# Kernel tuning notes

Hardware: AMD Instinct MI355X
Metric: run time of the kernel (lower is better)

Reference implementation:

```python
import jax, jax.numpy as jnp
import numpy as np

SPAN = 128
STRIDE = 4
LQ = 2048
LKV = 512
H = 16
DQK = 64
DV = 64
DQ = 1024
DOUT = 1024
T = SPAN // STRIDE  # table depth (rows of the sparse QK table)


def _tables():
    # Static precomputation mirroring the torch __init__ meshgrid logic.
    row, col = np.meshgrid(np.arange(T), np.arange(LQ), indexing='ij')
    qi_col = np.ceil((col - (SPAN - 1)) / STRIDE).astype(np.int64) + row  # kv index per (r, j)
    qi_row = -STRIDE * qi_col + col
    valid = (qi_row >= 0) & (qi_row < SPAN) & (qi_col >= 0) & (qi_col < LKV)
    kidx = np.clip(qi_col, 0, LKV - 1)  # clipped gather index; invalid slots masked later
    return jnp.asarray(kidx), jnp.asarray(valid)

KIDX, VALID = _tables()  # both [T, LQ]


def setup_inputs() -> dict:
    key = jax.random.key(0)
    ks = jax.random.split(key, 7)
    s = 0.02
    return {
        'q': jax.random.normal(ks[0], (2, LQ, DQ), jnp.float32),
        'k': jax.random.normal(ks[1], (2, LKV, DQ), jnp.float32),
        'v': jax.random.normal(ks[2], (2, LKV, DQ), jnp.float32),
        'Wq': jax.random.normal(ks[3], (DQ, H * DQK), jnp.float32) * s,
        'Wk': jax.random.normal(ks[4], (DQ, H * DQK), jnp.float32) * s,
        'Wv': jax.random.normal(ks[5], (DQ, H * DV), jnp.float32) * s,
        'Wo': jax.random.normal(ks[6], (H * DV, DOUT), jnp.float32) * s,
    }


def reference(q, k, v, Wq, Wk, Wv, Wo):
    B = q.shape[0]
    Q = (q @ Wq).reshape(B, LQ, H, DQK).transpose(0, 2, 1, 3)    # [B,H,LQ,DQK]
    K = (k @ Wk).reshape(B, LKV, H, DQK).transpose(0, 2, 1, 3)   # [B,H,LKV,DQK]
    V = (v @ Wv).reshape(B, LKV, H, DV).transpose(0, 2, 1, 3)    # [B,H,LKV,DV]

    # Gather K/V by the strided-span index table: [B,H,T,LQ,d]
    Kg = K[:, :, KIDX, :]
    Vg = V[:, :, KIDX, :]

    scores = jnp.einsum('bhjd,bhtjd->bhtj', Q, Kg) / np.float32(np.sqrt(DQK))
    scores = jnp.where(VALID, scores, -jnp.inf)
    probs = jax.nn.softmax(scores, axis=2)          # softmax over table rows (dim 2 in torch)
    probs = jnp.where(VALID, probs, 0.0)

    O = jnp.einsum('bhtj,bhtjd->bhjd', probs, Vg)   # [B,H,LQ,DV]
    O = O.transpose(0, 2, 1, 3).reshape(B, LQ, H * DV)
    return O @ Wo
```

## Files before the change

kernel.cpp:

```cpp
#include <hip/hip_runtime.h>
#include <hip/hip_bf16.h>

typedef __bf16 bf16x8 __attribute__((ext_vector_type(8)));
typedef float  f32x4  __attribute__((ext_vector_type(4)));
typedef unsigned short u16;
typedef unsigned int   u32;

__device__ __forceinline__ u16 f2b(float x) {
  __bf16 b = (__bf16)x;
  return __builtin_bit_cast(u16, b);
}

__device__ __forceinline__ void gload_lds16(const u16* g, u16* l) {
  __builtin_amdgcn_global_load_lds(
      (const __attribute__((address_space(1))) void*)g,
      (__attribute__((address_space(3))) void*)l, 16, 0, 0);
}

__device__ __forceinline__ void cvt8_store(u16* dst, float4 a, float4 b) {
  union { u16 u[8]; uint4 v; } r;
  r.u[0] = f2b(a.x); r.u[1] = f2b(a.y); r.u[2] = f2b(a.z); r.u[3] = f2b(a.w);
  r.u[4] = f2b(b.x); r.u[5] = f2b(b.y); r.u[6] = f2b(b.z); r.u[7] = f2b(b.w);
  *(uint4*)dst = r.v;
}

__device__ __forceinline__ void wtile_transpose(
    const float* __restrict__ W, u16* __restrict__ T, int rem, float* tile )
{
  int tx = threadIdx.x & 31, ty = threadIdx.x >> 5;
  int c0 = (rem & 31) << 5, r0 = (rem >> 5) << 5;
#pragma unroll
  for (int i = 0; i < 4; ++i)
    tile[(ty + i * 8) * 33 + tx] = W[(size_t)(r0 + ty + i * 8) * 1024 + c0 + tx];
  __syncthreads();
#pragma unroll
  for (int i = 0; i < 4; ++i)
    T[(size_t)(c0 + ty + i * 8) * 1024 + r0 + tx] = f2b(tile[tx * 33 + ty + i * 8]);
}

__global__ __launch_bounds__(256) void prep_kernel(
    const float* __restrict__ W0, const float* __restrict__ W1,
    const float* __restrict__ W2,
    u16* __restrict__ T0, u16* __restrict__ T1, u16* __restrict__ T2)
{
  __shared__ float tile[32 * 33];
  int t = blockIdx.x;
  int z = t >> 10, rem = t & 1023;
  const float* W = (z == 0) ? W0 : (z == 1) ? W1 : W2;
  u16* T = (z == 0) ? T0 : (z == 1) ? T1 : T2;
  wtile_transpose(W, T, rem, tile);
}

__device__ __forceinline__ void compute_step(
    const u16* asc, const u16* bsc, int lane, int wm, int wn, f32x4 (&acc)[4][4])
{
#pragma unroll
  for (int kk = 0; kk < 2; ++kk) {
    bf16x8 af[4], bfr[4];
    int colb = (kk << 6) + ((lane >> 4) << 4);
#pragma unroll
    for (int m = 0; m < 4; ++m) {
      int r = (wm << 6) + (m << 4) + (lane & 15);
      af[m] = *(const bf16x8*)((const char*)asc + (r << 7) + (colb ^ ((r & 7) << 4)));
    }
#pragma unroll
    for (int n = 0; n < 4; ++n) {
      int r = (wn << 6) + (n << 4) + (lane & 15);
      bfr[n] = *(const bf16x8*)((const char*)bsc + (r << 7) + (colb ^ ((r & 7) << 4)));
    }
#pragma unroll
    for (int m = 0; m < 4; ++m)
#pragma unroll
      for (int n = 0; n < 4; ++n)
        acc[m][n] = __builtin_amdgcn_mfma_f32_16x16x32_bf16(af[m], bfr[n], acc[m][n], 0, 0, 0);
  }
}

__device__ __forceinline__ void stage_b(const u16* gB, u16* bs, int wave, int K, int k0) {
#pragma unroll
  for (int i = 0; i < 4; ++i) {
    int rb = (wave << 5) + (i << 3);
    gload_lds16(gB + (size_t)(i << 3) * K + k0, bs + (rb << 6));
  }
}

template <int OUTF32>
__device__ __forceinline__ void cwrite(
    void* C, int N, int row0, int col0, int lane, int wm, int wn, f32x4 (&acc)[4][4])
{
  const int crow = (lane >> 4) << 2;
  const int ccol = lane & 15;
#pragma unroll
  for (int m = 0; m < 4; ++m) {
#pragma unroll
    for (int n = 0; n < 4; ++n) {
      int r = row0 + (wm << 6) + (m << 4) + crow;
      int c = col0 + (wn << 6) + (n << 4) + ccol;
#pragma unroll
      for (int reg = 0; reg < 4; ++reg) {
        if (OUTF32) ((float*)C)[(size_t)(r + reg) * N + c] = acc[m][n][reg];
        else        ((u16*)C)[(size_t)(r + reg) * N + c] = f2b(acc[m][n][reg]);
      }
    }
  }
}

template <int OUTF32>
__device__ __forceinline__ void gemm_core(
    const u16* __restrict__ A, const u16* __restrict__ Bt, void* __restrict__ C,
    int N, int K, int row0, int col0,
    u16* As0, u16* As1, u16* Bs0, u16* Bs1)
{
  const int tid = threadIdx.x;
  const int wave = tid >> 6, lane = tid & 63;
  const int wm = wave >> 1, wn = wave & 1;
  f32x4 acc[4][4] = {};

  const int srow = lane >> 3, sslot = lane & 7;
  const int scol = ((sslot ^ srow) << 3);
  const u16* gA = A + (size_t)(row0 + (wave << 5) + srow) * K + scol;
  const u16* gB = Bt + (size_t)(col0 + (wave << 5) + srow) * K + scol;

  stage_b(gA, As0, wave, K, 0);
  stage_b(gB, Bs0, wave, K, 0);
  __syncthreads();

  u16 *asc = As0, *bsc = Bs0, *asn = As1, *bsn = Bs1;
  for (int k0 = 0; k0 < K; k0 += 64) {
    if (k0 + 64 < K) {
      stage_b(gA, asn, wave, K, k0 + 64);
      stage_b(gB, bsn, wave, K, k0 + 64);
    }
    compute_step(asc, bsc, lane, wm, wn, acc);
    __syncthreads();
    u16* t_;
    t_ = asc; asc = asn; asn = t_;
    t_ = bsc; bsc = bsn; bsn = t_;
  }
  cwrite<OUTF32>(C, N, row0, col0, lane, wm, wn, acc);
}

__device__ __forceinline__ void gemm_core_f32a(
    const float* __restrict__ Af,
    const u16* __restrict__ Bt, u16* __restrict__ C,
    int N, int K, int row0, int col0,
    u16* As0, u16* As1, u16* Bs0, u16* Bs1)
{
  const int tid = threadIdx.x;
  const int wave = tid >> 6, lane = tid & 63;
  const int wm = wave >> 1, wn = wave & 1;
  f32x4 acc[4][4] = {};

  const int srow = lane >> 3, sslot = lane & 7;
  const int scol = ((sslot ^ srow) << 3);
  const float* gAf = Af + (size_t)((wave << 5) + srow) * K + scol;
  const u16*  gB  = Bt + (size_t)(col0 + (wave << 5) + srow) * K + scol;
  const int awbase = (lane << 3);

  float4 a0[4], a1[4];
#pragma unroll
  for (int i = 0; i < 4; ++i) {
    const float* g = gAf + (size_t)(i << 3) * K;
    a0[i] = *(const float4*)g; a1[i] = *(const float4*)(g + 4);
  }
  stage_b(gB, Bs0, wave, K, 0);
#pragma unroll
  for (int i = 0; i < 4; ++i)
    cvt8_store(As0 + (((wave << 5) + (i << 3)) << 6) + awbase, a0[i], a1[i]);
  __syncthreads();

  u16 *asc = As0, *bsc = Bs0, *asn = As1, *bsn = Bs1;
  for (int k0 = 0; k0 < K; k0 += 64) {
    const bool more = (k0 + 64) < K;
    if (more) {
#pragma unroll
      for (int i = 0; i < 4; ++i) {
        const float* g = gAf + (size_t)(i << 3) * K + (k0 + 64);
        a0[i] = *(const float4*)g; a1[i] = *(const float4*)(g + 4);
      }
      stage_b(gB, bsn, wave, K, k0 + 64);
    }
    compute_step(asc, bsc, lane, wm, wn, acc);
    __syncthreads();
    if (more) {
#pragma unroll
      for (int i = 0; i < 4; ++i)
        cvt8_store(asn + (((wave << 5) + (i << 3)) << 6) + awbase, a0[i], a1[i]);
    }
    __syncthreads();
    u16* t_;
    t_ = asc; asc = asn; asn = t_;
    t_ = bsc; bsc = bsn; bsn = t_;
  }
  cwrite<0>(C, N, row0, col0, lane, wm, wn, acc);
}

template <int OUTF32>
__global__ __launch_bounds__(256, 2) void gemm_bt_kernel(
    const u16* __restrict__ A, const u16* __restrict__ Bt, void* __restrict__ C,
    int M, int N, int K)
{
  __shared__ u16 As[2][8192];
  __shared__ u16 Bs[2][8192];
  int bid = blockIdx.x;
  int t = (bid & 7) * 32 + (bid >> 3);
  const int bx = t & 7, by = t >> 3;
  gemm_core<OUTF32>(A, Bt, C, N, K, by << 7, bx << 7, As[0], As[1], Bs[0], Bs[1]);
}

__global__ __launch_bounds__(256, 2) void proj_kernel(
    const float* __restrict__ q, const float* __restrict__ k, const float* __restrict__ v,
    const u16* __restrict__ Wqt, const u16* __restrict__ Wkt, const u16* __restrict__ Wvt,
    u16* __restrict__ Qp, u16* __restrict__ KVp)
{
  __shared__ u16 As[2][8192];
  __shared__ u16 Bs[2][8192];
  int bid = blockIdx.x;
  int t = (bid & 7) * 48 + (bid >> 3);
  const float* Af; const u16* Bt; u16* C; int row0, col0;
  if (t < 256) {
    row0 = (t >> 3) << 7; col0 = (t & 7) << 7;
    Af = q + (size_t)row0 * 1024; Bt = Wqt; C = Qp;
  } else {
    int t2 = t - 256;
    row0 = (t2 >> 3) << 7; col0 = (t2 & 7) << 7;
    if (row0 < 1024) { Af = k + (size_t)row0 * 1024; Bt = Wkt; }
    else             { Af = v + (size_t)(row0 - 1024) * 1024; Bt = Wvt; }
    C = KVp;
  }
  gemm_core_f32a(Af, Bt, C, 1024, 1024, row0, col0, As[0], As[1], Bs[0], Bs[1]);
}

#define VTP 56
#define PLP 72
__global__ __launch_bounds__(256) void attn_kernel(
    const u16* __restrict__ Qp, const u16* __restrict__ Kp,
    const u16* __restrict__ Vp, u16* __restrict__ Ob,
    const float* __restrict__ W3, u16* __restrict__ T3)
{
  __shared__ u16 Ql[64 * 64];
  __shared__ u16 Kl[48 * 64];
  __shared__ u16 Vt[64 * VTP + 64];
  __shared__ u16 Pl[64 * PLP];

  const int bid = blockIdx.x;
  if (bid >= 1024) {
    wtile_transpose(W3, T3, bid - 1024, (float*)Ql);
    return;
  }
  const int t = (bid & 7) * 128 + (bid >> 3);
  const int jt = t & 31, h = (t >> 5) & 15, b = t >> 9;
  const int j0 = jt << 6;
  const int kbase = (j0 - 124) >> 2;
  const int tid = threadIdx.x;
  const int wave = tid >> 6, lane = tid & 63;

  const int srow = lane >> 3, sslot = lane & 7;
  const int scol = ((sslot ^ srow) << 3);
  for (int g = wave; g < 8; g += 4) {
    int r = (g << 3) + srow;
    const u16* ga = Qp + (((size_t)(b * 2048 + j0 + r)) << 10) + (h << 6) + scol;
    gload_lds16(ga, &Ql[g << 9]);
  }
  for (int g = wave; g < 6; g += 4) {
    int r = (g << 3) + srow;
    int key = kbase + r;
    key = key < 0 ? 0 : (key > 511 ? 511 : key);
    const u16* gk = Kp + (((size_t)(b * 512 + key)) << 10) + (h << 6) + scol;
    gload_lds16(gk, &Kl[g << 9]);
  }
  for (int idx = tid; idx < 48 * 8; idx += 256) {
    int row = idx >> 3, seg = idx & 7;
    int key = kbase + row;
    key = key < 0 ? 0 : (key > 511 ? 511 : key);
    uint4 x = *(const uint4*)(Vp + (((size_t)(b * 512 + key)) << 10) + (h << 6) + (seg << 3));
    int d0 = seg << 3;
    Vt[(d0 + 0) * VTP + row] = (u16)(x.x);
    Vt[(d0 + 1) * VTP + row] = (u16)(x.x >> 16);
    Vt[(d0 + 2) * VTP + row] = (u16)(x.y);
    Vt[(d0 + 3) * VTP + row] = (u16)(x.y >> 16);
    Vt[(d0 + 4) * VTP + row] = (u16)(x.z);
    Vt[(d0 + 5) * VTP + row] = (u16)(x.z >> 16);
    Vt[(d0 + 6) * VTP + row] = (u16)(x.w);
    Vt[(d0 + 7) * VTP + row] = (u16)(x.w >> 16);
  }
  if (tid < 64) *(uint4*)&Vt[tid * VTP + 48] = make_uint4(0, 0, 0, 0);
  else if (tid < 72) *(uint4*)&Vt[64 * VTP + ((tid - 64) << 3)] = make_uint4(0, 0, 0, 0);
  __syncthreads();

  f32x4 sacc[3] = {};
  const int frow_a = (wave << 4) + (lane & 15);
#pragma unroll
  for (int kk = 0; kk < 2; ++kk) {
    int colb = (kk << 6) + ((lane >> 4) << 4);
    bf16x8 aq = *(const bf16x8*)((const char*)Ql + (frow_a << 7) + (colb ^ ((frow_a & 7) << 4)));
#pragma unroll
    for (int nt = 0; nt < 3; ++nt) {
      int rk = (nt << 4) + (lane & 15);
      bf16x8 bk = *(const bf16x8*)((const char*)Kl + (rk << 7) + (colb ^ ((rk & 7) << 4)));
      sacc[nt] = __builtin_amdgcn_mfma_f32_16x16x32_bf16(aq, bk, sacc[nt], 0, 0, 0);
    }
  }

  const int rof = (wave << 2) + (lane >> 4);
  const int cb0 = lane & 15;
  bool vld[3]; float sc[3][4];
#pragma unroll
  for (int nt = 0; nt < 3; ++nt) {
    int c = cb0 + (nt << 4);
    vld[nt] = ((unsigned)(c - rof) < 32u) && (kbase + c >= 0);
#pragma unroll
    for (int r = 0; r < 4; ++r) sc[nt][r] = sacc[nt][r] * 0.125f;
  }
  float mx[4], rs[4];
#pragma unroll
  for (int r = 0; r < 4; ++r) {
    float m = -3.0e38f;
#pragma unroll
    for (int nt = 0; nt < 3; ++nt) m = vld[nt] ? fmaxf(m, sc[nt][r]) : m;
    m = fmaxf(m, __shfl_xor(m, 1));
    m = fmaxf(m, __shfl_xor(m, 2));
    m = fmaxf(m, __shfl_xor(m, 4));
    m = fmaxf(m, __shfl_xor(m, 8));
    mx[r] = m;
  }
#pragma unroll
  for (int r = 0; r < 4; ++r) {
    float s = 0.f;
#pragma unroll
    for (int nt = 0; nt < 3; ++nt) {
      float e = vld[nt] ? __expf(sc[nt][r] - mx[r]) : 0.f;
      sc[nt][r] = e;
      s += e;
    }
    s += __shfl_xor(s, 1);
    s += __shfl_xor(s, 2);
    s += __shfl_xor(s, 4);
    s += __shfl_xor(s, 8);
    rs[r] = 1.f / s;
  }
#pragma unroll
  for (int r = 0; r < 4; ++r) {
    int jq = (wave << 4) + ((lane >> 4) << 2) + r;
#pragma unroll
    for (int nt = 0; nt < 3; ++nt)
      Pl[jq * PLP + cb0 + (nt << 4)] = f2b(sc[nt][r] * rs[r]);
    Pl[jq * PLP + 48 + cb0] = 0;
  }
  __syncthreads();

  f32x4 oacc[4] = {};
#pragma unroll
  for (int kk = 0; kk < 2; ++kk) {
    int koff = (kk << 5) + ((lane >> 4) << 3);
    bf16x8 ap = *(const bf16x8*)&Pl[frow_a * PLP + koff];
#pragma unroll
    for (int nt = 0; nt < 4; ++nt) {
      int dr = (nt << 4) + (lane & 15);
      bf16x8 bv = *(const bf16x8*)&Vt[dr * VTP + koff];
      oacc[nt] = __builtin_amdgcn_mfma_f32_16x16x32_bf16(ap, bv, oacc[nt], 0, 0, 0);
    }
  }

#pragma unroll
  for (int nt = 0; nt < 4; ++nt) {
    int d = (nt << 4) + (lane & 15);
#pragma unroll
    for (int r = 0; r < 4; ++r) {
      int jq = (wave << 4) + ((lane >> 4) << 2) + r;
      Ob[(((size_t)(b * 2048 + j0 + jq)) << 10) + (h << 6) + d] = f2b(oacc[nt][r]);
    }
  }
}

extern "C" void kernel_launch(void* const* d_in, const int* in_sizes, int n_in,
                              void* d_out, int out_size, void* d_ws, size_t ws_size,
                              hipStream_t stream) {
  const float* q  = (const float*)d_in[0];
  const float* k  = (const float*)d_in[1];
  const float* v  = (const float*)d_in[2];
  const float* Wq = (const float*)d_in[3];
  const float* Wk = (const float*)d_in[4];
  const float* Wv = (const float*)d_in[5];
  const float* Wo = (const float*)d_in[6];

  char* ws = (char*)d_ws;
  const size_t MB = 1u << 20;
  u16* Wqt = (u16*)(ws + 0 * MB);
  u16* Wkt = (u16*)(ws + 2 * MB);
  u16* Wvt = (u16*)(ws + 4 * MB);
  u16* Wot = (u16*)(ws + 6 * MB);
  u16* Qp  = (u16*)(ws + 8 * MB);
  u16* Kp  = (u16*)(ws + 16 * MB);
  u16* Vp  = (u16*)(ws + 18 * MB);
  u16* Ob  = (u16*)(ws + 20 * MB);

  prep_kernel<<<3072, 256, 0, stream>>>(Wq, Wk, Wv, Wqt, Wkt, Wvt);
  proj_kernel<<<384, 256, 0, stream>>>(q, k, v, Wqt, Wkt, Wvt, Qp, Kp);
  attn_kernel<<<2048, 256, 0, stream>>>(Qp, Kp, Vp, Ob, Wo, Wot);
  gemm_bt_kernel<1><<<256, 256, 0, stream>>>(Ob, Wot, d_out, 4096, 1024, 1024);
}
```

Before: 58.24 us.

## Enlarge attention tile to 128 queries and move Wo transpose into projection launch

The attention kernel now processes 128 query rows per block instead of 64, with each wave handling two 16-row MFMA tiles and using half of an 80-row K window. Q/K/V are staged once per larger tile, and the tail blocks that transpose Wo are moved from the attention launch into the projection launch. The aim is to cut redundant K/V loads across neighbouring tiles and overlap the Wo transpose with the projection GEMM. The cost is more LDS and registers per block and fewer blocks in the attention grid (512 instead of 1024 working blocks).

```diff
diff --git a/kernel.cpp b/kernel.cpp
--- a/kernel.cpp
+++ b/kernel.cpp
@@ -211,11 +211,16 @@
 __global__ __launch_bounds__(256, 2) void proj_kernel(
     const float* __restrict__ q, const float* __restrict__ k, const float* __restrict__ v,
     const u16* __restrict__ Wqt, const u16* __restrict__ Wkt, const u16* __restrict__ Wvt,
-    u16* __restrict__ Qp, u16* __restrict__ KVp)
+    u16* __restrict__ Qp, u16* __restrict__ KVp,
+    const float* __restrict__ W3, u16* __restrict__ T3)
 {
   __shared__ u16 As[2][8192];
   __shared__ u16 Bs[2][8192];
   int bid = blockIdx.x;
+  if (bid >= 384) {
+    wtile_transpose(W3, T3, bid - 384, (float*)As);
+    return;
+  }
   int t = (bid & 7) * 48 + (bid >> 3);
   const float* Af; const u16* Bt; u16* C; int row0, col0;
   if (t < 256) {
@@ -231,146 +236,153 @@
   gemm_core_f32a(Af, Bt, C, 1024, 1024, row0, col0, As[0], As[1], Bs[0], Bs[1]);
 }
 
-#define VTP 56
-#define PLP 72
+#define VTP2 88
+#define PLP2 72
 __global__ __launch_bounds__(256) void attn_kernel(
     const u16* __restrict__ Qp, const u16* __restrict__ Kp,
-    const u16* __restrict__ Vp, u16* __restrict__ Ob,
-    const float* __restrict__ W3, u16* __restrict__ T3)
-{
-  __shared__ u16 Ql[64 * 64];
-  __shared__ u16 Kl[48 * 64];
-  __shared__ u16 Vt[64 * VTP + 64];
-  __shared__ u16 Pl[64 * PLP];
+    const u16* __restrict__ Vp, u16* __restrict__ Ob)
+{
+  __shared__ u16 Ql[128 * 64];
+  __shared__ u16 Kl[80 * 64];
+  __shared__ u16 Vt[64 * VTP2];
+  __shared__ u16 Pl[128 * PLP2];
 
   const int bid = blockIdx.x;
-  if (bid >= 1024) {
-    wtile_transpose(W3, T3, bid - 1024, (float*)Ql);
-    return;
-  }
-  const int t = (bid & 7) * 128 + (bid >> 3);
-  const int jt = t & 31, h = (t >> 5) & 15, b = t >> 9;
-  const int j0 = jt << 6;
+  const int t = (bid & 7) * 64 + (bid >> 3);
+  const int jt2 = t & 15, h = (t >> 4) & 15, b = t >> 8;
+  const int j0 = jt2 << 7;
   const int kbase = (j0 - 124) >> 2;
   const int tid = threadIdx.x;
   const int wave = tid >> 6, lane = tid & 63;
 
   const int srow = lane >> 3, sslot = lane & 7;
   const int scol = ((sslot ^ srow) << 3);
-  for (int g = wave; g < 8; g += 4) {
+  for (int g = wave; g < 16; g += 4) {
     int r = (g << 3) + srow;
     const u16* ga = Qp + (((size_t)(b * 2048 + j0 + r)) << 10) + (h << 6) + scol;
     gload_lds16(ga, &Ql[g << 9]);
   }
-  for (int g = wave; g < 6; g += 4) {
+  for (int g = wave; g < 10; g += 4) {
     int r = (g << 3) + srow;
     int key = kbase + r;
     key = key < 0 ? 0 : (key > 511 ? 511 : key);
     const u16* gk = Kp + (((size_t)(b * 512 + key)) << 10) + (h << 6) + scol;
     gload_lds16(gk, &Kl[g << 9]);
   }
-  for (int idx = tid; idx < 48 * 8; idx += 256) {
+  for (int idx = tid; idx < 64 * 8; idx += 256) {
     int row = idx >> 3, seg = idx & 7;
     int key = kbase + row;
     key = key < 0 ? 0 : (key > 511 ? 511 : key);
     uint4 x = *(const uint4*)(Vp + (((size_t)(b * 512 + key)) << 10) + (h << 6) + (seg << 3));
     int d0 = seg << 3;
-    Vt[(d0 + 0) * VTP + row] = (u16)(x.x);
-    Vt[(d0 + 1) * VTP + row] = (u16)(x.x >> 16);
-    Vt[(d0 + 2) * VTP + row] = (u16)(x.y);
-    Vt[(d0 + 3) * VTP + row] = (u16)(x.y >> 16);
-    Vt[(d0 + 4) * VTP + row] = (u16)(x.z);
-    Vt[(d0 + 5) * VTP + row] = (u16)(x.z >> 16);
-    Vt[(d0 + 6) * VTP + row] = (u16)(x.w);
-    Vt[(d0 + 7) * VTP + row] = (u16)(x.w >> 16);
-  }
-  if (tid < 64) *(uint4*)&Vt[tid * VTP + 48] = make_uint4(0, 0, 0, 0);
-  else if (tid < 72) *(uint4*)&Vt[64 * VTP + ((tid - 64) << 3)] = make_uint4(0, 0, 0, 0);
+    Vt[(d0 + 0) * VTP2 + row] = (u16)(x.x);
+    Vt[(d0 + 1) * VTP2 + row] = (u16)(x.x >> 16);
+    Vt[(d0 + 2) * VTP2 + row] = (u16)(x.y);
+    Vt[(d0 + 3) * VTP2 + row] = (u16)(x.y >> 16);
+    Vt[(d0 + 4) * VTP2 + row] = (u16)(x.z);
+    Vt[(d0 + 5) * VTP2 + row] = (u16)(x.z >> 16);
+    Vt[(d0 + 6) * VTP2 + row] = (u16)(x.w);
+    Vt[(d0 + 7) * VTP2 + row] = (u16)(x.w >> 16);
+  }
+  if (tid < 128) {
+    int row = tid >> 1, q = tid & 1;
+    *(uint4*)&Vt[row * VTP2 + 64 + (q << 3)] = make_uint4(0, 0, 0, 0);
+  }
   __syncthreads();
 
-  f32x4 sacc[3] = {};
-  const int frow_a = (wave << 4) + (lane & 15);
+  const int s = wave >> 1;
+  const int cb0 = lane & 15;
+  const int frow0 = (wave << 5) + (lane & 15);
+
+  f32x4 sacc[2][4] = {};
 #pragma unroll
   for (int kk = 0; kk < 2; ++kk) {
     int colb = (kk << 6) + ((lane >> 4) << 4);
-    bf16x8 aq = *(const bf16x8*)((const char*)Ql + (frow_a << 7) + (colb ^ ((frow_a & 7) << 4)));
-#pragma unroll
-    for (int nt = 0; nt < 3; ++nt) {
-      int rk = (nt << 4) + (lane & 15);
+    bf16x8 aq[2];
+#pragma unroll
+    for (int mi = 0; mi < 2; ++mi) {
+      int fr = frow0 + (mi << 4);
+      aq[mi] = *(const bf16x8*)((const char*)Ql + (fr << 7) + (colb ^ ((fr & 7) << 4)));
+    }
+#pragma unroll
+    for (int nt = 0; nt < 4; ++nt) {
+      int rk = (s << 4) + (nt << 4) + (lane & 15);
       bf16x8 bk = *(const bf16x8*)((const char*)Kl + (rk << 7) + (colb ^ ((rk & 7) << 4)));
-      sacc[nt] = __builtin_amdgcn_mfma_f32_16x16x32_bf16(aq, bk, sacc[nt], 0, 0, 0);
-    }
-  }
-
-  const int rof = (wave << 2) + (lane >> 4);
-  const int cb0 = lane & 15;
-  bool vld[3]; float sc[3][4];
-#pragma unroll
-  for (int nt = 0; nt < 3; ++nt) {
-    int c = cb0 + (nt << 4);
-    vld[nt] = ((unsigned)(c - rof) < 32u) && (kbase + c >= 0);
-#pragma unroll
-    for (int r = 0; r < 4; ++r) sc[nt][r] = sacc[nt][r] * 0.125f;
-  }
-  float mx[4], rs[4];
-#pragma unroll
-  for (int r = 0; r < 4; ++r) {
-    float m = -3.0e38f;
-#pragma unroll
-    for (int nt = 0; nt < 3; ++nt) m = vld[nt] ? fmaxf(m, sc[nt][r]) : m;
-    m = fmaxf(m, __shfl_xor(m, 1));
-    m = fmaxf(m, __shfl_xor(m, 2));
-    m = fmaxf(m, __shfl_xor(m, 4));
-    m = fmaxf(m, __shfl_xor(m, 8));
-    mx[r] = m;
-  }
-#pragma unroll
-  for (int r = 0; r < 4; ++r) {
-    float s = 0.f;
-#pragma unroll
-    for (int nt = 0; nt < 3; ++nt) {
-      float e = vld[nt] ? __expf(sc[nt][r] - mx[r]) : 0.f;
-      sc[nt][r] = e;
-      s += e;
-    }
-    s += __shfl_xor(s, 1);
-    s += __shfl_xor(s, 2);
-    s += __shfl_xor(s, 4);
-    s += __shfl_xor(s, 8);
-    rs[r] = 1.f / s;
-  }
-#pragma unroll
-  for (int r = 0; r < 4; ++r) {
-    int jq = (wave << 4) + ((lane >> 4) << 2) + r;
-#pragma unroll
-    for (int nt = 0; nt < 3; ++nt)
-      Pl[jq * PLP + cb0 + (nt << 4)] = f2b(sc[nt][r] * rs[r]);
-    Pl[jq * PLP + 48 + cb0] = 0;
+#pragma unroll
+      for (int mi = 0; mi < 2; ++mi)
+        sacc[mi][nt] = __builtin_amdgcn_mfma_f32_16x16x32_bf16(aq[mi], bk, sacc[mi][nt], 0, 0, 0);
+    }
+  }
+
+#pragma unroll
+  for (int mi = 0; mi < 2; ++mi) {
+    const int rof = ((wave & 1) << 3) + (mi << 2) + (lane >> 4);
+    bool vld[4]; float sc[4][4];
+#pragma unroll
+    for (int nt = 0; nt < 4; ++nt) {
+      int c = (nt << 4) + cb0;
+      vld[nt] = ((unsigned)(c - rof) < 32u) && (kbase + (s << 4) + c >= 0);
+#pragma unroll
+      for (int r = 0; r < 4; ++r) sc[nt][r] = sacc[mi][nt][r] * 0.125f;
+    }
+#pragma unroll
+    for (int r = 0; r < 4; ++r) {
+      float m = -3.0e38f;
+#pragma unroll
+      for (int nt = 0; nt < 4; ++nt) m = vld[nt] ? fmaxf(m, sc[nt][r]) : m;
+      m = fmaxf(m, __shfl_xor(m, 1));
+      m = fmaxf(m, __shfl_xor(m, 2));
+      m = fmaxf(m, __shfl_xor(m, 4));
+      m = fmaxf(m, __shfl_xor(m, 8));
+      float ssum = 0.f;
+      float e[4];
+#pragma unroll
+      for (int nt = 0; nt < 4; ++nt) {
+        e[nt] = vld[nt] ? __expf(sc[nt][r] - m) : 0.f;
+        ssum += e[nt];
+      }
+      ssum += __shfl_xor(ssum, 1);
+      ssum += __shfl_xor(ssum, 2);
+      ssum += __shfl_xor(ssum, 4);
+      ssum += __shfl_xor(ssum, 8);
+      float rs = 1.f / ssum;
+      int jq = (wave << 5) + (mi << 4) + ((lane >> 4) << 2) + r;
+#pragma unroll
+      for (int nt = 0; nt < 4; ++nt)
+        Pl[jq * PLP2 + (nt << 4) + cb0] = f2b(e[nt] * rs);
+    }
   }
   __syncthreads();
 
-  f32x4 oacc[4] = {};
+  f32x4 oacc[2][4] = {};
 #pragma unroll
   for (int kk = 0; kk < 2; ++kk) {
     int koff = (kk << 5) + ((lane >> 4) << 3);
-    bf16x8 ap = *(const bf16x8*)&Pl[frow_a * PLP + koff];
+    bf16x8 ap[2];
+#pragma unroll
+    for (int mi = 0; mi < 2; ++mi)
+      ap[mi] = *(const bf16x8*)&Pl[(frow0 + (mi << 4)) * PLP2 + koff];
 #pragma unroll
     for (int nt = 0; nt < 4; ++nt) {
       int dr = (nt << 4) + (lane & 15);
-      bf16x8 bv = *(const bf16x8*)&Vt[dr * VTP + koff];
-      oacc[nt] = __builtin_amdgcn_mfma_f32_16x16x32_bf16(ap, bv, oacc[nt], 0, 0, 0);
-    }
-  }
-
-#pragma unroll
-  for (int nt = 0; nt < 4; ++nt) {
-    int d = (nt << 4) + (lane & 15);
-#pragma unroll
-    for (int r = 0; r < 4; ++r) {
-      int jq = (wave << 4) + ((lane >> 4) << 2) + r;
-      Ob[(((size_t)(b * 2048 + j0 + jq)) << 10) + (h << 6) + d] = f2b(oacc[nt][r]);
-    }
-  }
+      bf16x8 bv = *(const bf16x8*)&Vt[dr * VTP2 + (s << 4) + koff];
+#pragma unroll
+      for (int mi = 0; mi < 2; ++mi)
+        oacc[mi][nt] = __builtin_amdgcn_mfma_f32_16x16x32_bf16(ap[mi], bv, oacc[mi][nt], 0, 0, 0);
+    }
+  }
+
+#pragma unroll
+  for (int mi = 0; mi < 2; ++mi)
+#pragma unroll
+    for (int nt = 0; nt < 4; ++nt) {
+      int d = (nt << 4) + (lane & 15);
+#pragma unroll
+      for (int r = 0; r < 4; ++r) {
+        int jq = (wave << 5) + (mi << 4) + ((lane >> 4) << 2) + r;
+        Ob[(((size_t)(b * 2048 + j0 + jq)) << 10) + (h << 6) + d] = f2b(oacc[mi][nt][r]);
+      }
+    }
 }
 
 extern "C" void kernel_launch(void* const* d_in, const int* in_sizes, int n_in,
@@ -396,7 +408,7 @@
   u16* Ob  = (u16*)(ws + 20 * MB);
 
   prep_kernel<<<3072, 256, 0, stream>>>(Wq, Wk, Wv, Wqt, Wkt, Wvt);
-  proj_kernel<<<384, 256, 0, stream>>>(q, k, v, Wqt, Wkt, Wvt, Qp, Kp);
-  attn_kernel<<<2048, 256, 0, stream>>>(Qp, Kp, Vp, Ob, Wo, Wot);
+  proj_kernel<<<1408, 256, 0, stream>>>(q, k, v, Wqt, Wkt, Wvt, Qp, Kp, Wo, Wot);
+  attn_kernel<<<512, 256, 0, stream>>>(Qp, Kp, Vp, Ob);
   gemm_bt_kernel<1><<<256, 256, 0, stream>>>(Ob, Wot, d_out, 4096, 1024, 1024);
 }
```

New measurement: 58.08 us, median of 2. About the same (-0.3%).
